# Optimization experiments

Measured on AMD Instinct MI355X. Metric: run time of the kernel, lower is better.

Reference implementation:

```python
import jax, jax.numpy as jnp
import numpy as np

N = 100000  # nodes
E = 1600000  # edges
D_IN = 64
D_H = 64


def _sage_conv(x, src, dst, w_l, b_l, w_r):
    """PyG SAGEConv (mean aggr): lin_l(mean_j x_j) + lin_r(x_i).
    w_l, w_r: [out, in]; b_l: [out]."""
    # scatter-mean of source features onto target nodes
    msg_sum = jax.ops.segment_sum(x[src], dst, num_segments=N)  # [N, in]
    cnt = jax.ops.segment_sum(jnp.ones((src.shape[0],), x.dtype), dst, num_segments=N)
    mean = msg_sum / jnp.maximum(cnt, 1.0)[:, None]
    return mean @ w_l.T + b_l + x @ w_r.T


def setup_inputs() -> dict:
    key = jax.random.key(0)
    ks = jax.random.split(key, 8)
    x = jax.random.normal(ks[0], (N, D_IN), dtype=jnp.float32)
    edge_index = jax.random.randint(ks[1], (2, E), 0, N, dtype=jnp.int64)
    s = 1.0 / np.sqrt(D_IN)
    w_l1 = jax.random.uniform(ks[2], (D_H, D_IN), jnp.float32, -s, s)
    b_l1 = jnp.zeros((D_H,), jnp.float32)
    w_r1 = jax.random.uniform(ks[3], (D_H, D_IN), jnp.float32, -s, s)
    s2 = 1.0 / np.sqrt(D_H)
    w_l2 = jax.random.uniform(ks[4], (D_H, D_H), jnp.float32, -s2, s2)
    b_l2 = jnp.zeros((D_H,), jnp.float32)
    w_r2 = jax.random.uniform(ks[5], (D_H, D_H), jnp.float32, -s2, s2)
    return {"x": x, "edge_index": edge_index,
            "w_l1": w_l1, "b_l1": b_l1, "w_r1": w_r1,
            "w_l2": w_l2, "b_l2": b_l2, "w_r2": w_r2}


def reference(x, edge_index, w_l1, b_l1, w_r1, w_l2, b_l2, w_r2):
    src, dst = edge_index[0], edge_index[1]
    h = jax.nn.relu(_sage_conv(x, src, dst, w_l1, b_l1, w_r1))
    out = _sage_conv(h, src, dst, w_l2, b_l2, w_r2)
    return out
```

## Files before the change

kernel.cpp:

```cpp
#include <hip/hip_runtime.h>

#define N_NODES 100000
#define N_EDGES 1600000
#define D 64

#define BSHIFT 7
#define BNODES (1 << BSHIFT)
#define NB ((N_NODES + BNODES - 1) / BNODES)
#define PB 256
#define TILE ((N_EDGES + PB - 1) / PB)
#define CAP 2432
#define MAXB 4096
#define CAST_BLKS 512
#define QBLKS ((N_NODES * D / 4 + 1023) / 1024)
#define HPARTS (N_NODES / 16)

typedef __attribute__((ext_vector_type(8))) short short8;
typedef __attribute__((ext_vector_type(4))) float float4v;
typedef __attribute__((ext_vector_type(2))) unsigned uint2v;
typedef __attribute__((ext_vector_type(4))) unsigned uint4v;

__device__ __forceinline__ unsigned short f2bf(float f) {
    unsigned u = __float_as_uint(f);
    u = (u + 0x7fffu + ((u >> 16) & 1u)) >> 16;
    return (unsigned short)u;
}
__device__ __forceinline__ unsigned cvtpk(float a, float b) {
    unsigned r;
    asm("v_cvt_pk_bf16_f32 %0, %1, %2" : "=v"(r) : "v"(a), "v"(b));
    return r;
}

__device__ __forceinline__ float4 bf16x4_to_f4(uint2 v) {
    float4 r;
    r.x = __uint_as_float(v.x << 16);
    r.y = __uint_as_float(v.x & 0xffff0000u);
    r.z = __uint_as_float(v.y << 16);
    r.w = __uint_as_float(v.y & 0xffff0000u);
    return r;
}

__global__ __launch_bounds__(1024) void front(const float* __restrict__ x,
                                              unsigned short* __restrict__ xb,
                                              float* __restrict__ partial,
                                              const int* __restrict__ src,
                                              const int* __restrict__ dst,
                                              int* __restrict__ gcnt,
                                              int* __restrict__ part) {
    __shared__ float red[16];
    __shared__ int hist[NB];

    if (blockIdx.x < CAST_BLKS) {
        float m = 0.0f;
        int stride = CAST_BLKS * 1024;
        for (int i = blockIdx.x * 1024 + threadIdx.x; i < N_NODES * D / 4; i += stride) {
            float4 v = ((const float4*)x)[i];
            ushort4 o;
            o.x = f2bf(v.x); o.y = f2bf(v.y); o.z = f2bf(v.z); o.w = f2bf(v.w);
            ((ushort4*)xb)[i] = o;
            m = fmaxf(m, fmaxf(fmaxf(fabsf(v.x), fabsf(v.y)), fmaxf(fabsf(v.z), fabsf(v.w))));
        }
        for (int off = 32; off >= 1; off >>= 1) m = fmaxf(m, __shfl_xor(m, off, 64));
        if ((threadIdx.x & 63) == 0) red[threadIdx.x >> 6] = m;
        __syncthreads();
        if (threadIdx.x == 0) {
            float mm = 0.0f;
#pragma unroll
            for (int w = 0; w < 16; ++w) mm = fmaxf(mm, red[w]);
            partial[blockIdx.x] = mm;
        }
        return;
    }

    int bid = blockIdx.x - CAST_BLKS;
    for (int i = threadIdx.x; i < NB; i += 1024) hist[i] = 0;
    __syncthreads();

    int lo = bid * TILE;
    int hi = min(lo + TILE, N_EDGES);

    unsigned pk[7];
    int bk[7];
#pragma unroll
    for (int k = 0; k < 7; ++k) {
        int e = lo + threadIdx.x + k * 1024;
        if (e < hi) {
            int dd = dst[e];
            int ss = src[e];
            int b = dd >> BSHIFT;
            pk[k] = ((unsigned)ss << BSHIFT) | (unsigned)(dd & (BNODES - 1));
            bk[k] = b;
            atomicAdd(&hist[b], 1);
        } else {
            bk[k] = -1;
        }
    }
    __syncthreads();

    for (int b = threadIdx.x; b < NB; b += 1024) {
        int h = hist[b];
        if (h) hist[b] = b * CAP + atomicAdd(&gcnt[b], h);
    }
    __syncthreads();

#pragma unroll
    for (int k = 0; k < 7; ++k) {
        if (bk[k] >= 0) {
            int p = atomicAdd(&hist[bk[k]], 1);
            part[p] = (int)pk[k];
        }
    }
}

__device__ __forceinline__ void quant_body(int i, const unsigned short* __restrict__ inb,
                                           unsigned char* __restrict__ out8, float s) {
    uint2 v = ((const uint2*)inb)[i];
    float4 f = bf16x4_to_f4(v);
    int q0 = min(127, max(-127, __float2int_rn(f.x * s))) + 128;
    int q1 = min(127, max(-127, __float2int_rn(f.y * s))) + 128;
    int q2 = min(127, max(-127, __float2int_rn(f.z * s))) + 128;
    int q3 = min(127, max(-127, __float2int_rn(f.w * s))) + 128;
    ((unsigned*)out8)[i] = (unsigned)q0 | ((unsigned)q1 << 8) |
                           ((unsigned)q2 << 16) | ((unsigned)q3 << 24);
}

__device__ __forceinline__ float fold_partials(const float* __restrict__ partial,
                                               int n, float* red, float* bc) {
    int tid = threadIdx.x;
    float m = 0.0f;
    for (int i = tid; i < n; i += 1024) m = fmaxf(m, partial[i]);
    for (int off = 32; off >= 1; off >>= 1) m = fmaxf(m, __shfl_xor(m, off, 64));
    if ((tid & 63) == 0) red[tid >> 6] = m;
    __syncthreads();
    if (tid == 0) {
        float mm = 0.0f;
#pragma unroll
        for (int w = 0; w < 16; ++w) mm = fmaxf(mm, red[w]);
        *bc = mm;
    }
    __syncthreads();
    return *bc;
}

__global__ __launch_bounds__(1024) void back(const int* __restrict__ gcnt,
                                             const int* __restrict__ part,
                                             int* __restrict__ row_ptr,
                                             int* __restrict__ sorted_src,
                                             const unsigned short* __restrict__ xb,
                                             unsigned char* __restrict__ x8,
                                             const float* __restrict__ partial,
                                             unsigned* __restrict__ amax_store,
                                             const float* __restrict__ wl1,
                                             const float* __restrict__ wr1,
                                             unsigned short* __restrict__ wb1,
                                             const float* __restrict__ wl2,
                                             const float* __restrict__ wr2,
                                             unsigned short* __restrict__ wb2) {
    __shared__ int in_buf[MAXB];
    __shared__ int out_buf[MAXB];
    __shared__ int hist[BNODES];
    __shared__ int exs[BNODES];
    __shared__ int cursor[BNODES];
    __shared__ float red[16];
    __shared__ float bc;

    int tid = threadIdx.x;

    if (blockIdx.x >= NB + QBLKS) {
        int i = (blockIdx.x - NB - QBLKS) * 1024 + tid;
        int j = i & 8191;
        int o = j >> 7, kk = j & 127;
        if (i < 8192) {
            float v = (kk < D) ? wl1[o * D + kk] : wr1[o * D + (kk - D)];
            wb1[j] = f2bf(v);
        } else {
            float v = (kk < D) ? wl2[o * D + kk] : wr2[o * D + (kk - D)];
            wb2[j] = f2bf(v);
        }
        return;
    }

    if (blockIdx.x >= NB) {
        float A = fold_partials(partial, CAST_BLKS, red, &bc);
        if (blockIdx.x == NB && tid == 0) *amax_store = __float_as_uint(A);
        float s = (A > 0.0f) ? 127.0f / A : 0.0f;
        int i = (blockIdx.x - NB) * 1024 + tid;
        if (i < N_NODES * D / 4) quant_body(i, xb, x8, s);
        return;
    }

    int k = blockIdx.x;

    int v = (tid < NB) ? gcnt[tid] : 0;
    int val = v;
    in_buf[tid] = val;
    __syncthreads();
    for (int off = 1; off < 1024; off <<= 1) {
        int u = (tid >= off) ? in_buf[tid - off] : 0;
        __syncthreads();
        val += u;
        in_buf[tid] = val;
        __syncthreads();
    }
    int base  = (k > 0) ? in_buf[k - 1] : 0;
    int count = gcnt[k];
    int src0  = k * CAP;
    __syncthreads();

    for (int i = tid; i < BNODES; i += 1024) hist[i] = 0;
    __syncthreads();

    for (int i = tid; i < count; i += 1024) {
        int w = part[src0 + i];
        in_buf[i] = w;
        atomicAdd(&hist[w & (BNODES - 1)], 1);
    }
    __syncthreads();
    if (tid < 64) {
        int a = hist[2 * tid], b = hist[2 * tid + 1];
        int s = a + b, incl = s;
        for (int off = 1; off < 64; off <<= 1) {
            int t = __shfl_up(incl, off, 64);
            if (tid >= off) incl += t;
        }
        int excl = incl - s;
        exs[2 * tid] = excl;
        exs[2 * tid + 1] = excl + a;
    }
    __syncthreads();
    if (tid < BNODES) {
        int node = k * BNODES + tid;
        if (node < N_NODES) row_ptr[node] = base + exs[tid];
        cursor[tid] = exs[tid];
    }
    if (tid == 0 && k == NB - 1) row_ptr[N_NODES] = N_EDGES;
    __syncthreads();
    for (int i = tid; i < count; i += 1024) {
        int w = in_buf[i];
        int r = atomicAdd(&cursor[w & (BNODES - 1)], 1);
        out_buf[r] = w >> BSHIFT;
    }
    __syncthreads();
    for (int i = tid; i < count; i += 1024)
        sorted_src[base + i] = out_buf[i];
}

__global__ __launch_bounds__(1024) void quant8f(const unsigned short* __restrict__ inb,
                                                unsigned char* __restrict__ out8,
                                                const float* __restrict__ partial,
                                                unsigned* __restrict__ amax_store) {
    __shared__ float red[16];
    __shared__ float bc;
    float A = fold_partials(partial, HPARTS, red, &bc);
    if (blockIdx.x == 0 && threadIdx.x == 0) *amax_store = __float_as_uint(A);
    float s = (A > 0.0f) ? 127.0f / A : 0.0f;
    int i = blockIdx.x * 1024 + threadIdx.x;
    if (i < N_NODES * D / 4) quant_body(i, inb, out8, s);
}

#define ACCW(w, kk) { aLo[kk] += (w) & 0x00FF00FFu; \
                      aHi[kk] += __builtin_amdgcn_perm(0u, (w), 0x04030401u); }
#define ACC4(v) { ACCW((v).x, 0) ACCW((v).y, 1) ACCW((v).z, 2) ACCW((v).w, 3) }

__global__ __launch_bounds__(512, 8) void sage8(
    const int* __restrict__ row_ptr, const int* __restrict__ nbr,
    const unsigned char* __restrict__ tab8,
    const unsigned short* __restrict__ selfb,
    const unsigned* __restrict__ amax_bits,
    const unsigned short* __restrict__ wb,
    const float* __restrict__ b_l,
    float* __restrict__ out,
    unsigned short* __restrict__ outb,
    float* __restrict__ hpart,
    int apply_relu)
{
    __shared__ unsigned short a_s[16][136];
    __shared__ float st[16][68];
    __shared__ float bias[D];
    __shared__ float wred[4];

    int tid = threadIdx.x;
    if (tid < D) bias[tid] = b_l[tid];

    int wave = tid >> 6;
    int lane = tid & 63;
    int nsel = lane >> 5;
    int l32  = lane & 31;
    int g    = l32 >> 2;
    int c    = l32 & 3;
    int arow = wave * 2 + nsel;
    int node = blockIdx.x * 16 + arow;

    float A  = __uint_as_float(*amax_bits);
    float gs = A * (1.0f / 127.0f);

    int begin = row_ptr[node];
    int end   = row_ptr[node + 1];

    uint2v xv = {0, 0};
    if (l32 < 16)
        xv = __builtin_nontemporal_load((const uint2v*)&selfb[(size_t)node * D + 4 * l32]);

    unsigned c16 = (unsigned)(c << 4);
    unsigned aLo[4] = {0, 0, 0, 0};
    unsigned aHi[4] = {0, 0, 0, 0};
    for (int base = begin; base < end; base += 32) {
        int m = end - base; if (m > 32) m = 32;
        int id = (l32 < m) ? __builtin_nontemporal_load(&nbr[base + l32]) : 0;
        int s0 = __shfl(id, nsel * 32 + g,      64);
        int s1 = __shfl(id, nsel * 32 + 8 + g,  64);
        int s2 = __shfl(id, nsel * 32 + 16 + g, 64);
        int s3 = __shfl(id, nsel * 32 + 24 + g, 64);
        bool a0 = (g < m), a1 = (8 + g < m), a2 = (16 + g < m), a3 = (24 + g < m);
        uint4 v0, v1, v2, v3;
        if (a0) v0 = *(const uint4*)(tab8 + ((((unsigned)s0) << 6) | c16));
        if (a1) v1 = *(const uint4*)(tab8 + ((((unsigned)s1) << 6) | c16));
        if (a2) v2 = *(const uint4*)(tab8 + ((((unsigned)s2) << 6) | c16));
        if (a3) v3 = *(const uint4*)(tab8 + ((((unsigned)s3) << 6) | c16));
        if (a0) { ACC4(v0) }
        if (a1) { ACC4(v1) }
        if (a2) { ACC4(v2) }
        if (a3) { ACC4(v3) }
    }

#pragma unroll
    for (int off = 4; off <= 16; off <<= 1) {
#pragma unroll
        for (int k = 0; k < 4; ++k) {
            aLo[k] += (unsigned)__shfl_xor((int)aLo[k], off, 64);
            aHi[k] += (unsigned)__shfl_xor((int)aHi[k], off, 64);
        }
    }

    int   deg  = end - begin;
    float invd = 1.0f / fmaxf((float)deg, 1.0f);
    float sc   = gs * invd;
    float nofs = -128.0f * (float)deg * sc;

    {
        unsigned lo01 = (g & 2) ? aLo[1] : aLo[0];
        unsigned lo23 = (g & 2) ? aLo[3] : aLo[2];
        unsigned wLo  = (g & 4) ? lo23 : lo01;
        unsigned hi01 = (g & 2) ? aHi[1] : aHi[0];
        unsigned hi23 = (g & 2) ? aHi[3] : aHi[2];
        unsigned wHi  = (g & 4) ? hi23 : hi01;
        int sh = (g & 1) << 4;
        float d0 = (float)((wLo >> sh) & 0xFFFFu);
        float d1 = (float)((wHi >> sh) & 0xFFFFu);
        float f0 = fmaf(d0, sc, nofs);
        float f1 = fmaf(d1, sc, nofs);
        *(unsigned*)&a_s[arow][16 * c + 2 * g] = cvtpk(f0, f1);
    }
    if (l32 < 16)
        *(uint2v*)&a_s[arow][64 + 4 * l32] = xv;
    __syncthreads();

    if (wave < 4) {
        int quad = lane >> 4;
        int cc   = lane & 15;

        float4v acc = {0.f, 0.f, 0.f, 0.f};
#pragma unroll
        for (int kk = 0; kk < 4; ++kk) {
            short8 af = *(const short8*)&a_s[cc][kk * 32 + quad * 8];
            short8 bf = *(const short8*)(wb + (size_t)(wave * 16 + cc) * 128 + kk * 32 + quad * 8);
            acc = __builtin_amdgcn_mfma_f32_16x16x32_bf16(af, bf, acc, 0, 0, 0);
        }

        int o = wave * 16 + cc;
        float bv = bias[o];
        float vv[4];
#pragma unroll
        for (int r = 0; r < 4; ++r) {
            float v = acc[r] + bv;
            if (apply_relu) v = fmaxf(v, 0.0f);
            vv[r] = v;
            st[quad * 4 + r][o] = v;
        }
        if (hpart) {
            float m = fmaxf(fmaxf(fabsf(vv[0]), fabsf(vv[1])),
                            fmaxf(fabsf(vv[2]), fabsf(vv[3])));
            for (int off = 32; off >= 1; off >>= 1) m = fmaxf(m, __shfl_xor(m, off, 64));
            if (lane == 0) wred[wave] = m;
        }
    }
    __syncthreads();

    if (wave >= 4) {
        int idx = tid - 256;
        if (outb) {
            if (idx < 128) {
                int row = idx >> 3, c8 = idx & 7;
                const float* p = &st[row][c8 * 8];
                float4v f0 = *(const float4v*)p;
                float4v f1 = *(const float4v*)(p + 4);
                uint4v q;
                q[0] = cvtpk(f0[0], f0[1]); q[1] = cvtpk(f0[2], f0[3]);
                q[2] = cvtpk(f1[0], f1[1]); q[3] = cvtpk(f1[2], f1[3]);
                __builtin_nontemporal_store(q,
                    (uint4v*)&outb[((size_t)(blockIdx.x * 16 + row)) * D + 8 * c8]);
            }
        } else {
            int row = idx >> 4, c4 = idx & 15;
            uint4v q = *(const uint4v*)&st[row][c4 * 4];
            __builtin_nontemporal_store(q,
                (uint4v*)&out[((size_t)(blockIdx.x * 16 + row)) * D + 4 * c4]);
        }
        if (hpart && idx == 0)
            hpart[blockIdx.x] = fmaxf(fmaxf(wred[0], wred[1]), fmaxf(wred[2], wred[3]));
    }
}

extern "C" void kernel_launch(void* const* d_in, const int* in_sizes, int n_in,
                              void* d_out, int out_size, void* d_ws, size_t ws_size,
                              hipStream_t stream) {
    const float* x    = (const float*)d_in[0];
    const int*   ei   = (const int*)d_in[1];
    const float* w_l1 = (const float*)d_in[2];
    const float* b_l1 = (const float*)d_in[3];
    const float* w_r1 = (const float*)d_in[4];
    const float* w_l2 = (const float*)d_in[5];
    const float* b_l2 = (const float*)d_in[6];
    const float* w_r2 = (const float*)d_in[7];
    float* out = (float*)d_out;

    const int* src = ei;
    const int* dst = ei + N_EDGES;

    unsigned* scales   = (unsigned*)d_ws;
    int* gcnt          = (int*)d_ws + 4;
    int* row_ptr       = gcnt + NB;
    int* part          = row_ptr + 100004;
    int* sorted_src    = part + NB * CAP;
    unsigned short* xb = (unsigned short*)(sorted_src + N_EDGES);
    unsigned short* hb = xb + (size_t)N_NODES * D;
    unsigned char* x8  = (unsigned char*)(hb + (size_t)N_NODES * D);
    unsigned char* h8  = x8 + (size_t)N_NODES * D;
    unsigned short* wb1 = (unsigned short*)(h8 + (size_t)N_NODES * D);
    unsigned short* wb2 = wb1 + D * 2 * D;
    float* partA       = (float*)(wb2 + D * 2 * D);

    (void)hipMemsetAsync(d_ws, 0, 16 + NB * sizeof(int), stream);

    front<<<dim3(CAST_BLKS + PB), dim3(1024), 0, stream>>>(x, xb, partA,
                                                           src, dst, gcnt, part);
    back<<<dim3(NB + QBLKS + 16), dim3(1024), 0, stream>>>(gcnt, part,
                                                           row_ptr, sorted_src,
                                                           xb, x8, partA, &scales[0],
                                                           w_l1, w_r1, wb1,
                                                           w_l2, w_r2, wb2);

    dim3 lblk(512);
    dim3 lgrid(N_NODES / 16);
    sage8<<<lgrid, lblk, 0, stream>>>(row_ptr, sorted_src, x8, xb,
                                      &scales[0], wb1, b_l1,
                                      (float*)nullptr, hb, partA, 1);
    quant8f<<<dim3(QBLKS), dim3(1024), 0, stream>>>(hb, h8, partA, &scales[1]);
    sage8<<<lgrid, lblk, 0, stream>>>(row_ptr, sorted_src, h8, hb,
                                      &scales[1], wb2, b_l2,
                                      out, (unsigned short*)nullptr,
                                      (float*)nullptr, 0);
}
```

Baseline: 214.8 us.

## Stage edge partition in shared memory for coalesced global scatter

```diff
diff --git a/kernel.cpp b/kernel.cpp
--- a/kernel.cpp
+++ b/kernel.cpp
@@ -49,11 +49,17 @@
                                               int* __restrict__ part) {
     __shared__ float red[16];
     __shared__ int hist[NB];
+    __shared__ int lcur[NB];
+    __shared__ int gbase[NB];
+    __shared__ int ebuf[TILE];
+    __shared__ int gtgt[TILE];
+
+    int tid = threadIdx.x;
 
     if (blockIdx.x < CAST_BLKS) {
         float m = 0.0f;
         int stride = CAST_BLKS * 1024;
-        for (int i = blockIdx.x * 1024 + threadIdx.x; i < N_NODES * D / 4; i += stride) {
+        for (int i = blockIdx.x * 1024 + tid; i < N_NODES * D / 4; i += stride) {
             float4 v = ((const float4*)x)[i];
             ushort4 o;
             o.x = f2bf(v.x); o.y = f2bf(v.y); o.z = f2bf(v.z); o.w = f2bf(v.w);
@@ -61,9 +67,9 @@
             m = fmaxf(m, fmaxf(fmaxf(fabsf(v.x), fabsf(v.y)), fmaxf(fabsf(v.z), fabsf(v.w))));
         }
         for (int off = 32; off >= 1; off >>= 1) m = fmaxf(m, __shfl_xor(m, off, 64));
-        if ((threadIdx.x & 63) == 0) red[threadIdx.x >> 6] = m;
+        if ((tid & 63) == 0) red[tid >> 6] = m;
         __syncthreads();
-        if (threadIdx.x == 0) {
+        if (tid == 0) {
             float mm = 0.0f;
 #pragma unroll
             for (int w = 0; w < 16; ++w) mm = fmaxf(mm, red[w]);
@@ -73,18 +79,17 @@
     }
 
     int bid = blockIdx.x - CAST_BLKS;
-    for (int i = threadIdx.x; i < NB; i += 1024) hist[i] = 0;
+    for (int i = tid; i < NB; i += 1024) hist[i] = 0;
     __syncthreads();
 
     int lo = bid * TILE;
-    int hi = min(lo + TILE, N_EDGES);
 
     unsigned pk[7];
     int bk[7];
 #pragma unroll
     for (int k = 0; k < 7; ++k) {
-        int e = lo + threadIdx.x + k * 1024;
-        if (e < hi) {
+        int e = lo + tid + k * 1024;
+        if (tid + k * 1024 < TILE) {
             int dd = dst[e];
             int ss = src[e];
             int b = dd >> BSHIFT;
@@ -97,19 +102,38 @@
     }
     __syncthreads();
 
-    for (int b = threadIdx.x; b < NB; b += 1024) {
-        int h = hist[b];
-        if (h) hist[b] = b * CAP + atomicAdd(&gcnt[b], h);
+    int h = (tid < NB) ? hist[tid] : 0;
+    if (tid < NB)
+        gbase[tid] = tid * CAP + (h ? atomicAdd(&gcnt[tid], h) : 0);
+    int val = h;
+    gtgt[tid] = val;
+    __syncthreads();
+    for (int off = 1; off < 1024; off <<= 1) {
+        int u = (tid >= off) ? gtgt[tid - off] : 0;
+        __syncthreads();
+        val += u;
+        gtgt[tid] = val;
+        __syncthreads();
+    }
+    if (tid < NB) {
+        hist[tid] = val - h;
+        lcur[tid] = val - h;
     }
     __syncthreads();
 
 #pragma unroll
     for (int k = 0; k < 7; ++k) {
         if (bk[k] >= 0) {
-            int p = atomicAdd(&hist[bk[k]], 1);
-            part[p] = (int)pk[k];
-        }
-    }
+            int b = bk[k];
+            int p = atomicAdd(&lcur[b], 1);
+            ebuf[p] = (int)pk[k];
+            gtgt[p] = gbase[b] + (p - hist[b]);
+        }
+    }
+    __syncthreads();
+
+    for (int i = tid; i < TILE; i += 1024)
+        part[gtgt[i]] = ebuf[i];
 }
 
 __device__ __forceinline__ void quant_body(int i, const unsigned short* __restrict__ inb,
```

After: 210.3 us. 1.02x faster.
